# Optimization experiments

Hardware: AMD Instinct MI355X
Metric: run time of the kernel (lower is better)

The kernel has to match this reference:

```python
import jax, jax.numpy as jnp
import numpy as np

# 47 skeleton edges (parent, child) from getSkeletalModelStructure()
EDGES = np.array([
    (0, 1), (1, 2), (2, 3), (3, 29), (1, 5), (5, 6), (6, 8), (8, 9), (8, 13),
    (8, 17), (8, 21), (8, 25), (9, 10), (10, 11), (11, 12), (13, 14), (14, 15),
    (15, 16), (17, 18), (18, 19), (19, 20), (21, 22), (22, 23), (23, 24),
    (25, 26), (26, 27), (27, 28), (29, 30), (29, 34), (29, 38), (29, 42),
    (29, 46), (30, 31), (31, 32), (32, 33), (34, 35), (35, 36), (36, 37),
    (38, 39), (39, 40), (40, 41), (42, 43), (43, 44), (44, 45), (46, 47),
    (47, 48), (48, 49)], dtype=np.int32)

N_JOINTS = 50
N_EDGES = 47


def _length_direct(pose):
    # pose: [B, T, 151]; drop counter channel, view as joints
    B, T = pose.shape[0], pose.shape[1]
    p = pose[..., :-1].reshape(B, T, N_JOINTS, 3)
    diff = p[:, :, EDGES[:, 0], :] - p[:, :, EDGES[:, 1], :]   # [B, T, 47, 3]
    length = jnp.linalg.norm(diff, axis=-1)                      # [B, T, 47]
    eps = jnp.finfo(pose.dtype).tiny
    direct = diff / (length + eps)[..., None]                    # [B, T, 47, 3]
    # torch stacks each [B,T,3] edge dir along dim=-1 -> [B,T,3,47], then reshapes
    directs = jnp.transpose(direct, (0, 1, 3, 2)).reshape(B, T, N_EDGES * 3)
    return length, directs


def setup_inputs() -> dict:
    key = jax.random.key(0)
    k1, k2 = jax.random.split(key)
    B, T, D = 128, 1024, 151
    preds = jax.random.normal(k1, (B, T, D), dtype=jnp.float32)
    targets = jax.random.normal(k2, (B, T, D), dtype=jnp.float32)
    return {"preds": preds, "targets": targets}


def reference(preds, targets):
    target_pad = 0.0
    mask = (targets != target_pad).astype(preds.dtype)           # [B, T, 151]
    preds_m = preds * mask
    targets_m = targets * mask
    _, preds_dir = _length_direct(preds_m)
    _, targets_dir = _length_direct(targets_m)
    preds_dir = preds_dir * mask[:, :, :N_EDGES * 3]
    targets_dir = targets_dir * mask[:, :, :N_EDGES * 3]
    # cfg: loss='l1' (mean abs), vel_loss='mse' (mean square), loss_scale=1.0
    l1 = jnp.mean(jnp.abs(preds_m - targets_m))
    vel_mse = jnp.mean(jnp.square(preds_dir - targets_dir))
    return l1 + 0.1 * vel_mse
```

## Files before the change

### kernel.cpp

```cpp
#include <hip/hip_runtime.h>


#define N_ROWS   (128 * 1024)
#define ROW      151
#define N_EDGES  47
#define GRID     2048
#define BLOCK    256
#define TILE_ROWS 16
#define TILES_PER_BLOCK 4
#define TILE_DWORDS (TILE_ROWS * ROW)
#define TILE_F4 (TILE_DWORDS / 4)
#define N_TASKS (TILE_ROWS * N_EDGES)

__constant__ unsigned int c_edge[N_EDGES] = {
    (0*3)|(1*3<<16),  (1*3)|(2*3<<16),  (2*3)|(3*3<<16),  (3*3)|(29*3<<16),
    (1*3)|(5*3<<16),  (5*3)|(6*3<<16),  (6*3)|(8*3<<16),  (8*3)|(9*3<<16),
    (8*3)|(13*3<<16), (8*3)|(17*3<<16), (8*3)|(21*3<<16), (8*3)|(25*3<<16),
    (9*3)|(10*3<<16), (10*3)|(11*3<<16),(11*3)|(12*3<<16),(13*3)|(14*3<<16),
    (14*3)|(15*3<<16),(15*3)|(16*3<<16),(17*3)|(18*3<<16),(18*3)|(19*3<<16),
    (19*3)|(20*3<<16),(21*3)|(22*3<<16),(22*3)|(23*3<<16),(23*3)|(24*3<<16),
    (25*3)|(26*3<<16),(26*3)|(27*3<<16),(27*3)|(28*3<<16),(29*3)|(30*3<<16),
    (29*3)|(34*3<<16),(29*3)|(38*3<<16),(29*3)|(42*3<<16),(29*3)|(46*3<<16),
    (30*3)|(31*3<<16),(31*3)|(32*3<<16),(32*3)|(33*3<<16),(34*3)|(35*3<<16),
    (35*3)|(36*3<<16),(36*3)|(37*3<<16),(38*3)|(39*3<<16),(39*3)|(40*3<<16),
    (40*3)|(41*3<<16),(42*3)|(43*3<<16),(43*3)|(44*3<<16),(44*3)|(45*3<<16),
    (46*3)|(47*3<<16),(47*3)|(48*3<<16),(48*3)|(49*3<<16)};

__global__ __launch_bounds__(BLOCK) void reg_loss_main(
        const float* __restrict__ preds, const float* __restrict__ targets,
        float* __restrict__ wsL, float* __restrict__ wsV) {
    __shared__ float pmS[TILE_ROWS][ROW + 1];
    __shared__ float tmS[TILE_ROWS][ROW + 1];
    __shared__ float redL[4], redV[4];

    const int t = threadIdx.x;
    const int lane = t & 63;
    const int wave = t >> 6;

    float l1 = 0.f;
    float vel = 0.f;

    for (int tile = 0; tile < TILES_PER_BLOCK; ++tile) {
        const long long tileIdx = (long long)blockIdx.x * TILES_PER_BLOCK + tile;
        const float4* __restrict__ p4 =
            (const float4*)(preds + tileIdx * TILE_DWORDS);
        const float4* __restrict__ t4 =
            (const float4*)(targets + tileIdx * TILE_DWORDS);

        if (tile) __syncthreads();

#pragma unroll
        for (int k = 0; k < 3; ++k) {
            int i = t + k * BLOCK;
            if (i < TILE_F4) {
                float4 pv = p4[i];
                float4 tv = t4[i];
                float pe[4] = {pv.x, pv.y, pv.z, pv.w};
                float te[4] = {tv.x, tv.y, tv.z, tv.w};
                int d0 = i * 4;
#pragma unroll
                for (int j = 0; j < 4; ++j) {
                    int d = d0 + j;
                    int r = d / ROW;
                    int c = d - r * ROW;
                    float tt = te[j];
                    float pm = (tt != 0.f) ? pe[j] : 0.f;
                    l1 += fabsf(pm - tt);
                    pmS[r][c] = pm;
                    tmS[r][c] = tt;
                }
            }
        }
        __syncthreads();

#pragma unroll
        for (int k = 0; k < 3; ++k) {
            int task = t + k * BLOCK;
            if (task < N_TASKS) {
                int r = task / N_EDGES;
                int e = task - r * N_EDGES;
                unsigned int pk = c_edge[e];
                int pi = pk & 0xffff;
                int ci = pk >> 16;
                float pdx = pmS[r][pi]     - pmS[r][ci];
                float pdy = pmS[r][pi + 1] - pmS[r][ci + 1];
                float pdz = pmS[r][pi + 2] - pmS[r][ci + 2];
                float tdx = tmS[r][pi]     - tmS[r][ci];
                float tdy = tmS[r][pi + 1] - tmS[r][ci + 1];
                float tdz = tmS[r][pi + 2] - tmS[r][ci + 2];
                const float eps = 1.17549435e-38f;
                float pinv = 1.f / (sqrtf(pdx*pdx + pdy*pdy + pdz*pdz) + eps);
                float tinv = 1.f / (sqrtf(tdx*tdx + tdy*tdy + tdz*tdz) + eps);
                float dx = pdx * pinv - tdx * tinv;
                float dy = pdy * pinv - tdy * tinv;
                float dz = pdz * pinv - tdz * tinv;
                float m0 = (tmS[r][e]      != 0.f) ? 1.f : 0.f;
                float m1 = (tmS[r][47 + e] != 0.f) ? 1.f : 0.f;
                float m2 = (tmS[r][94 + e] != 0.f) ? 1.f : 0.f;
                vel += m0 * dx * dx + m1 * dy * dy + m2 * dz * dz;
            }
        }
    }

#pragma unroll
    for (int off = 32; off > 0; off >>= 1) {
        l1  += __shfl_down(l1, off);
        vel += __shfl_down(vel, off);
    }
    if (lane == 0) { redL[wave] = l1; redV[wave] = vel; }
    __syncthreads();
    if (t == 0) {
        wsL[blockIdx.x] = redL[0] + redL[1] + redL[2] + redL[3];
        wsV[blockIdx.x] = redV[0] + redV[1] + redV[2] + redV[3];
    }
}

__global__ __launch_bounds__(BLOCK) void reg_loss_finalize(
        const float* __restrict__ wsL, const float* __restrict__ wsV,
        float* __restrict__ out) {
    __shared__ double rl[4], rv[4];
    const int t = threadIdx.x;
    const int lane = t & 63;
    const int wave = t >> 6;
    double L = 0.0, V = 0.0;
    for (int k = t; k < GRID; k += BLOCK) { L += wsL[k]; V += wsV[k]; }
#pragma unroll
    for (int off = 32; off > 0; off >>= 1) {
        L += __shfl_down(L, off);
        V += __shfl_down(V, off);
    }
    if (lane == 0) { rl[wave] = L; rv[wave] = V; }
    __syncthreads();
    if (t == 0) {
        double Ls = rl[0] + rl[1] + rl[2] + rl[3];
        double Vs = rv[0] + rv[1] + rv[2] + rv[3];
        out[0] = (float)(Ls / ((double)N_ROWS * 151.0)
                       + 0.1 * (Vs / ((double)N_ROWS * 141.0)));
    }
}

extern "C" void kernel_launch(void* const* d_in, const int* in_sizes, int n_in,
                              void* d_out, int out_size, void* d_ws, size_t ws_size,
                              hipStream_t stream) {
    const float* preds   = (const float*)d_in[0];
    const float* targets = (const float*)d_in[1];
    float* wsL = (float*)d_ws;
    float* wsV = wsL + GRID;
    float* out = (float*)d_out;

    reg_loss_main<<<GRID, BLOCK, 0, stream>>>(preds, targets, wsL, wsV);
    reg_loss_finalize<<<1, BLOCK, 0, stream>>>(wsL, wsV, out);
}
```

Before: 189.2 us.

## Give each wave its own row slice with interleaved pred/target shared memory

Each wave now independently loads and processes 4 rows in a private shared-memory slice, so the block-wide barriers between the load and edge phases go away. Preds and targets are stored interleaved as (pred, target) pairs, which allows float4 stores and float2 loads instead of scalar accesses with per-element divisions. The grid grows to 8192 blocks with one pass each, in place of the 4-tile loop. This trades larger finalize work and less latency hiding per wave for fewer syncs and cheaper indexing.

Measured after the change: 183.0 us. -3.3%, faster.

```diff
diff --git a/kernel.cpp b/kernel.cpp
--- a/kernel.cpp
+++ b/kernel.cpp
@@ -4,101 +4,90 @@
 #define N_ROWS   (128 * 1024)
 #define ROW      151
 #define N_EDGES  47
-#define GRID     2048
+#define GRID     8192
 #define BLOCK    256
-#define TILE_ROWS 16
-#define TILES_PER_BLOCK 4
-#define TILE_DWORDS (TILE_ROWS * ROW)
-#define TILE_F4 (TILE_DWORDS / 4)
-#define N_TASKS (TILE_ROWS * N_EDGES)
+#define ROWS_PER_WAVE 4
+#define WAVE_DWORDS (ROWS_PER_WAVE * ROW)
+#define WAVE_F4 (WAVE_DWORDS / 4)
+#define WAVE_TASKS (ROWS_PER_WAVE * N_EDGES)
+#define S_STRIDE (ROW * 2)
 
-__constant__ unsigned int c_edge[N_EDGES] = {
-    (0*3)|(1*3<<16),  (1*3)|(2*3<<16),  (2*3)|(3*3<<16),  (3*3)|(29*3<<16),
-    (1*3)|(5*3<<16),  (5*3)|(6*3<<16),  (6*3)|(8*3<<16),  (8*3)|(9*3<<16),
-    (8*3)|(13*3<<16), (8*3)|(17*3<<16), (8*3)|(21*3<<16), (8*3)|(25*3<<16),
-    (9*3)|(10*3<<16), (10*3)|(11*3<<16),(11*3)|(12*3<<16),(13*3)|(14*3<<16),
-    (14*3)|(15*3<<16),(15*3)|(16*3<<16),(17*3)|(18*3<<16),(18*3)|(19*3<<16),
-    (19*3)|(20*3<<16),(21*3)|(22*3<<16),(22*3)|(23*3<<16),(23*3)|(24*3<<16),
-    (25*3)|(26*3<<16),(26*3)|(27*3<<16),(27*3)|(28*3<<16),(29*3)|(30*3<<16),
-    (29*3)|(34*3<<16),(29*3)|(38*3<<16),(29*3)|(42*3<<16),(29*3)|(46*3<<16),
-    (30*3)|(31*3<<16),(31*3)|(32*3<<16),(32*3)|(33*3<<16),(34*3)|(35*3<<16),
-    (35*3)|(36*3<<16),(36*3)|(37*3<<16),(38*3)|(39*3<<16),(39*3)|(40*3<<16),
-    (40*3)|(41*3<<16),(42*3)|(43*3<<16),(43*3)|(44*3<<16),(44*3)|(45*3<<16),
-    (46*3)|(47*3<<16),(47*3)|(48*3<<16),(48*3)|(49*3<<16)};
+#define E(p, c) ((unsigned)((p) * 6) | ((unsigned)((c) * 6) << 16))
+__constant__ unsigned c_edge[N_EDGES] = {
+    E(0,1),  E(1,2),  E(2,3),  E(3,29), E(1,5),  E(5,6),  E(6,8),  E(8,9),
+    E(8,13), E(8,17), E(8,21), E(8,25), E(9,10), E(10,11),E(11,12),E(13,14),
+    E(14,15),E(15,16),E(17,18),E(18,19),E(19,20),E(21,22),E(22,23),E(23,24),
+    E(25,26),E(26,27),E(27,28),E(29,30),E(29,34),E(29,38),E(29,42),E(29,46),
+    E(30,31),E(31,32),E(32,33),E(34,35),E(35,36),E(36,37),E(38,39),E(39,40),
+    E(40,41),E(42,43),E(43,44),E(44,45),E(46,47),E(47,48),E(48,49)};
 
 __global__ __launch_bounds__(BLOCK) void reg_loss_main(
         const float* __restrict__ preds, const float* __restrict__ targets,
         float* __restrict__ wsL, float* __restrict__ wsV) {
-    __shared__ float pmS[TILE_ROWS][ROW + 1];
-    __shared__ float tmS[TILE_ROWS][ROW + 1];
+    __shared__ float S[4][ROWS_PER_WAVE * S_STRIDE];
     __shared__ float redL[4], redV[4];
 
     const int t = threadIdx.x;
     const int lane = t & 63;
     const int wave = t >> 6;
+    float* __restrict__ Sw = S[wave];
+    float4* __restrict__ S4 = (float4*)Sw;
+
+    const long long base = ((long long)blockIdx.x * 4 + wave) * WAVE_DWORDS;
+    const float4* __restrict__ p4 = (const float4*)(preds + base);
+    const float4* __restrict__ t4 = (const float4*)(targets + base);
 
     float l1 = 0.f;
     float vel = 0.f;
 
-    for (int tile = 0; tile < TILES_PER_BLOCK; ++tile) {
-        const long long tileIdx = (long long)blockIdx.x * TILES_PER_BLOCK + tile;
-        const float4* __restrict__ p4 =
-            (const float4*)(preds + tileIdx * TILE_DWORDS);
-        const float4* __restrict__ t4 =
-            (const float4*)(targets + tileIdx * TILE_DWORDS);
-
-        if (tile) __syncthreads();
+#pragma unroll
+    for (int k = 0; k < 3; ++k) {
+        int i = lane + k * 64;
+        if (i < WAVE_F4) {
+            float4 pv = p4[i];
+            float4 tv = t4[i];
+            float4 pm;
+            pm.x = (tv.x != 0.f) ? pv.x : 0.f;
+            pm.y = (tv.y != 0.f) ? pv.y : 0.f;
+            pm.z = (tv.z != 0.f) ? pv.z : 0.f;
+            pm.w = (tv.w != 0.f) ? pv.w : 0.f;
+            l1 += fabsf(pm.x - tv.x) + fabsf(pm.y - tv.y)
+                + fabsf(pm.z - tv.z) + fabsf(pm.w - tv.w);
+            float4 a = {pm.x, tv.x, pm.y, tv.y};
+            float4 b = {pm.z, tv.z, pm.w, tv.w};
+            S4[i * 2]     = a;
+            S4[i * 2 + 1] = b;
+        }
+    }
 
 #pragma unroll
-        for (int k = 0; k < 3; ++k) {
-            int i = t + k * BLOCK;
-            if (i < TILE_F4) {
-                float4 pv = p4[i];
-                float4 tv = t4[i];
-                float pe[4] = {pv.x, pv.y, pv.z, pv.w};
-                float te[4] = {tv.x, tv.y, tv.z, tv.w};
-                int d0 = i * 4;
-#pragma unroll
-                for (int j = 0; j < 4; ++j) {
-                    int d = d0 + j;
-                    int r = d / ROW;
-                    int c = d - r * ROW;
-                    float tt = te[j];
-                    float pm = (tt != 0.f) ? pe[j] : 0.f;
-                    l1 += fabsf(pm - tt);
-                    pmS[r][c] = pm;
-                    tmS[r][c] = tt;
-                }
-            }
-        }
-        __syncthreads();
-
-#pragma unroll
-        for (int k = 0; k < 3; ++k) {
-            int task = t + k * BLOCK;
-            if (task < N_TASKS) {
-                int r = task / N_EDGES;
-                int e = task - r * N_EDGES;
-                unsigned int pk = c_edge[e];
-                int pi = pk & 0xffff;
-                int ci = pk >> 16;
-                float pdx = pmS[r][pi]     - pmS[r][ci];
-                float pdy = pmS[r][pi + 1] - pmS[r][ci + 1];
-                float pdz = pmS[r][pi + 2] - pmS[r][ci + 2];
-                float tdx = tmS[r][pi]     - tmS[r][ci];
-                float tdy = tmS[r][pi + 1] - tmS[r][ci + 1];
-                float tdz = tmS[r][pi + 2] - tmS[r][ci + 2];
-                const float eps = 1.17549435e-38f;
-                float pinv = 1.f / (sqrtf(pdx*pdx + pdy*pdy + pdz*pdz) + eps);
-                float tinv = 1.f / (sqrtf(tdx*tdx + tdy*tdy + tdz*tdz) + eps);
-                float dx = pdx * pinv - tdx * tinv;
-                float dy = pdy * pinv - tdy * tinv;
-                float dz = pdz * pinv - tdz * tinv;
-                float m0 = (tmS[r][e]      != 0.f) ? 1.f : 0.f;
-                float m1 = (tmS[r][47 + e] != 0.f) ? 1.f : 0.f;
-                float m2 = (tmS[r][94 + e] != 0.f) ? 1.f : 0.f;
-                vel += m0 * dx * dx + m1 * dy * dy + m2 * dz * dz;
-            }
+    for (int k = 0; k < 3; ++k) {
+        int task = lane + k * 64;
+        if (task < WAVE_TASKS) {
+            int r = task / N_EDGES;
+            int e = task - r * N_EDGES;
+            const float* __restrict__ R = Sw + r * S_STRIDE;
+            unsigned pk = c_edge[e];
+            int pi = pk & 0xffff;
+            int ci = pk >> 16;
+            float2 px = *(const float2*)(R + pi);
+            float2 py = *(const float2*)(R + pi + 2);
+            float2 pz = *(const float2*)(R + pi + 4);
+            float2 cx = *(const float2*)(R + ci);
+            float2 cy = *(const float2*)(R + ci + 2);
+            float2 cz = *(const float2*)(R + ci + 4);
+            float pdx = px.x - cx.x, pdy = py.x - cy.x, pdz = pz.x - cz.x;
+            float tdx = px.y - cx.y, tdy = py.y - cy.y, tdz = pz.y - cz.y;
+            const float eps = 1.17549435e-38f;
+            float pinv = 1.f / (sqrtf(pdx*pdx + pdy*pdy + pdz*pdz) + eps);
+            float tinv = 1.f / (sqrtf(tdx*tdx + tdy*tdy + tdz*tdz) + eps);
+            float dx = pdx * pinv - tdx * tinv;
+            float dy = pdy * pinv - tdy * tinv;
+            float dz = pdz * pinv - tdz * tinv;
+            float m0 = (R[e * 2 + 1]        != 0.f) ? 1.f : 0.f;
+            float m1 = (R[(47 + e) * 2 + 1] != 0.f) ? 1.f : 0.f;
+            float m2 = (R[(94 + e) * 2 + 1] != 0.f) ? 1.f : 0.f;
+            vel += m0 * dx * dx + m1 * dy * dy + m2 * dz * dz;
         }
     }
 
```
